# Optimization experiments

Hardware: AMD Instinct MI355X
Metric: run time of the kernel (lower is better)

The kernel has to match this reference:

```python
import jax, jax.numpy as jnp
import numpy as np

B, C_IN, C_OUT = 4, 64, 64
Z = H = W = 64
MZ = MH = MW = 16
R = 16


def setup_inputs() -> dict:
    key = jax.random.key(0)
    ks = jax.random.split(key, 12)
    p = lambda k, s: jax.random.normal(k, s, jnp.float32) * 0.02
    return {
        "x": jax.random.normal(ks[0], (B, C_IN, Z, H, W), jnp.float32),
        "U_in": p(ks[1], (C_IN, R)),
        "U_out": p(ks[2], (C_OUT, R)),
        "U_z": p(ks[3], (MZ, R)),
        "U_h": p(ks[4], (MH, R)),
        "U_w": p(ks[5], (MW, R)),
        "U_z2": p(ks[6], (MZ, R)),
        "U_h2": p(ks[7], (MH, R)),
        "core_r": p(ks[8], (R, R, R, R, R)),
        "core_i": p(ks[9], (R, R, R, R, R)),
        "core2_r": p(ks[10], (R, R, R, R, R)),
        "core2_i": p(ks[11], (R, R, R, R, R)),
    }


def _reconstruct(U_in, U_out, Uz, Uh, Uw, core):
    # Original: einsum('ir,or,zr,hr,wr,abcde->iozwh', ..., core).
    # core's a..e indices are summed independently of the shared r index,
    # so the weight equals the CP outer product scaled by core.sum().
    c = jnp.complex64
    w = jnp.einsum('ir,or,zr,hr,wr->iozwh',
                   U_in.astype(c), U_out.astype(c), Uz.astype(c),
                   Uh.astype(c), Uw.astype(c))
    return w * jnp.sum(core)  # (in, out, mz, mw, mh)


def reference(x, U_in, U_out, U_z, U_h, U_w, U_z2, U_h2,
              core_r, core_i, core2_r, core2_i):
    mz, mh, mw = U_z.shape[0], U_h.shape[0], U_w.shape[0]
    b, _, z, h, w = x.shape
    core = core_r + 1j * core_i
    core2 = core2_r + 1j * core2_i

    x_ft = jnp.fft.rfftn(x, axes=(-3, -2, -1))  # (B, Cin, Z, H, W//2+1) c64
    w1 = _reconstruct(U_in, U_out, U_z, U_h, U_w, core)
    w2 = _reconstruct(U_in, U_out, U_z2, U_h2, U_w, core2)

    lo = jnp.einsum('bixyz,ioxyz->boxyz', x_ft[:, :, :mz, :mh, :mw], w1)
    hi = jnp.einsum('bixyz,ioxyz->boxyz', x_ft[:, :, -mz:, :mh, :mw], w2)

    out_ft = jnp.zeros((b, U_out.shape[0], z, h, w // 2 + 1), jnp.complex64)
    out_ft = out_ft.at[:, :, :mz, :mh, :mw].set(lo)
    out_ft = out_ft.at[:, :, -mz:, :mh, :mw].set(hi)

    return jnp.fft.irfftn(out_ft, s=(z, h, w), axes=(-3, -2, -1)).astype(jnp.float32)
```

## Files before the change

### kernel.cpp

```cpp
#include <hip/hip_runtime.h>

#define TWOPI 6.28318530717958647692f

constexpr float COSQ[17] = {
  1.0f, 0.995184727f, 0.980785280f, 0.956940336f, 0.923879533f,
  0.881921264f, 0.831469612f, 0.773010453f, 0.707106781f,
  0.634393284f, 0.555570233f, 0.471396737f, 0.382683432f,
  0.290284677f, 0.195090322f, 0.098017140f, 0.0f
};
__host__ __device__ constexpr float cos64f(int k) {
  k &= 63;
  return (k <= 16) ? COSQ[k] : (k < 32) ? -COSQ[32 - k]
       : (k <= 48) ? -COSQ[k - 32] : COSQ[64 - k];
}
__host__ __device__ constexpr float sin64f(int k) { return cos64f(k + 48); }


__global__ __launch_bounds__(256) void k_core_partial(
    const float* __restrict__ a0, const float* __restrict__ a1,
    const float* __restrict__ a2, const float* __restrict__ a3,
    float* __restrict__ partial) {
  const float* p = blockIdx.y == 0 ? a0 : blockIdx.y == 1 ? a1
                 : blockIdx.y == 2 ? a2 : a3;
  const float4* p4 = (const float4*)p;
  float s = 0.f;
  int base = blockIdx.x * 4096 + threadIdx.x;
  #pragma unroll
  for (int i = 0; i < 16; ++i) {
    float4 v = p4[base + i * 256];
    s += (v.x + v.y) + (v.z + v.w);
  }
  __shared__ float red[256];
  red[threadIdx.x] = s;
  __syncthreads();
  for (int off = 128; off; off >>= 1) {
    if (threadIdx.x < off) red[threadIdx.x] += red[threadIdx.x + off];
    __syncthreads();
  }
  if (threadIdx.x == 0) partial[blockIdx.y * 64 + blockIdx.x] = red[0];
}

__global__ __launch_bounds__(256) void k_fwd_wh(const float* __restrict__ x,
                                                float2* __restrict__ A2) {
  __shared__ float2 T[4][64][17];
  int wave = threadIdx.x >> 6, lane = threadIdx.x & 63;
  int plane = blockIdx.x * 4 + wave;
  const float* xp = x + (size_t)plane * 4096 + lane;
  float cre[16], cim[16];
  {
    float x0 = xp[0], x32 = xp[32 * 64];
    #pragma unroll
    for (int hf = 0; hf < 16; ++hf) {
      cre[hf] = x0 + ((hf & 1) ? -x32 : x32);
      cim[hf] = 0.f;
    }
  }
  #pragma unroll
  for (int h = 1; h < 32; ++h) {
    float va = xp[h * 64], vb = xp[(64 - h) * 64];
    float u = va + vb, d = va - vb;
    #pragma unroll
    for (int hf = 0; hf < 16; ++hf) {
      cre[hf] = fmaf(u, cos64f(h * hf), cre[hf]);
      cim[hf] = fmaf(d, -sin64f(h * hf), cim[hf]);
    }
  }
  #pragma unroll
  for (int hf = 0; hf < 16; ++hf)
    T[wave][lane][hf] = make_float2(cre[hf], cim[hf]);
  __syncthreads();
  int hf = lane & 15, wq = lane >> 4;
  float2 rot[4], CS[4], acc[4];
  float2 T0 = T[wave][0][hf], T32 = T[wave][32][hf];
  #pragma unroll
  for (int j = 0; j < 4; ++j) {
    int wf = wq + 4 * j;
    float s, c;
    sincosf((TWOPI / 64.f) * (float)wf, &s, &c);
    rot[j] = make_float2(c, s);
    CS[j] = make_float2(c, s);
    float sgn = (wf & 1) ? -1.f : 1.f;
    acc[j] = make_float2(T0.x + sgn * T32.x, T0.y + sgn * T32.y);
  }
  #pragma unroll 4
  for (int w = 1; w < 32; ++w) {
    float2 a = T[wave][w][hf], b2 = T[wave][64 - w][hf];
    float Sr = a.x + b2.x, Si = a.y + b2.y;
    float Dr = a.x - b2.x, Di = a.y - b2.y;
    #pragma unroll
    for (int j = 0; j < 4; ++j) {
      float C = CS[j].x, Sn = CS[j].y;
      acc[j].x = fmaf(Sr, C, fmaf(Di, Sn, acc[j].x));
      acc[j].y = fmaf(Si, C, fmaf(-Dr, Sn, acc[j].y));
      float nC = C * rot[j].x - Sn * rot[j].y;
      CS[j].y = fmaf(C, rot[j].y, Sn * rot[j].x);
      CS[j].x = nC;
    }
  }
  float2* dst = A2 + (size_t)plane * 256 + lane;
  #pragma unroll
  for (int j = 0; j < 4; ++j) dst[j * 64] = acc[j];
}

__global__ __launch_bounds__(256) void k_proj(const float2* __restrict__ A2,
                                              float2* __restrict__ P,
                                              const float* __restrict__ U_in,
                                              const float* __restrict__ partial,
                                              float* __restrict__ S) {
  if (blockIdx.x == 0 && threadIdx.x < 4) {
    float s = 0.f;
    for (int j = 0; j < 64; ++j) s += partial[threadIdx.x * 64 + j];
    S[threadIdx.x] = s;
  }
  __shared__ float sU[1024];
  int t = threadIdx.x;
  #pragma unroll
  for (int i = 0; i < 4; ++i) sU[t + 256 * i] = U_in[t + 256 * i];
  __syncthreads();
  int b = blockIdx.x >> 6, z = blockIdx.x & 63;
  const float2* src = A2 + (((size_t)b * 64) * 64 + z) * 256 + t;
  float2 acc[16];
  #pragma unroll
  for (int r = 0; r < 16; ++r) acc[r] = make_float2(0.f, 0.f);
  for (int c = 0; c < 64; ++c) {
    float2 v = src[(size_t)c * 16384];
    #pragma unroll
    for (int r = 0; r < 16; ++r) {
      float u = sU[c * 16 + r];
      acc[r].x = fmaf(v.x, u, acc[r].x);
      acc[r].y = fmaf(v.y, u, acc[r].y);
    }
  }
  float2* dst = P + (((size_t)b * 16) * 64 + z) * 256 + t;
  #pragma unroll
  for (int r = 0; r < 16; ++r) dst[(size_t)r * 16384] = acc[r];
}

template <int HALF>
__device__ __forceinline__ void inv_z_body(const float* __restrict__ gr,
                                           const float* __restrict__ gi,
                                           float2* __restrict__ dst) {
  if (HALF == 0) {
    {
      float sr = 0.f, si = 0.f;
      #pragma unroll
      for (int k = 0; k < 32; ++k) { sr += gr[k]; si += gi[k]; }
      dst[0] = make_float2(sr, si);
    }
    #pragma unroll
    for (int z = 1; z <= 16; ++z) {
      float Ar = 0.f, Ai = 0.f, Br = 0.f, Bi = 0.f;
      #pragma unroll
      for (int k = 0; k < 32; ++k) {
        const int f = (k < 16) ? k : (k + 32);
        const float c = cos64f(z * f), s = sin64f(z * f);
        Ar = fmaf(gr[k], c, Ar); Ai = fmaf(gi[k], c, Ai);
        Br = fmaf(gr[k], s, Br); Bi = fmaf(gi[k], s, Bi);
      }
      dst[z * 256] = make_float2(Ar - Bi, Ai + Br);
      dst[(64 - z) * 256] = make_float2(Ar + Bi, Ai - Br);
    }
  } else {
    {
      float sr = 0.f, si = 0.f;
      #pragma unroll
      for (int k = 0; k < 32; ++k) {
        if (k & 1) { sr -= gr[k]; si -= gi[k]; }
        else       { sr += gr[k]; si += gi[k]; }
      }
      dst[32 * 256] = make_float2(sr, si);
    }
    #pragma unroll
    for (int z = 17; z < 32; ++z) {
      float Ar = 0.f, Ai = 0.f, Br = 0.f, Bi = 0.f;
      #pragma unroll
      for (int k = 0; k < 32; ++k) {
        const int f = (k < 16) ? k : (k + 32);
        const float c = cos64f(z * f), s = sin64f(z * f);
        Ar = fmaf(gr[k], c, Ar); Ai = fmaf(gi[k], c, Ai);
        Br = fmaf(gr[k], s, Br); Bi = fmaf(gi[k], s, Bi);
      }
      dst[z * 256] = make_float2(Ar - Bi, Ai + Br);
      dst[(64 - z) * 256] = make_float2(Ar + Bi, Ai - Br);
    }
  }
}

__global__ __launch_bounds__(256) void k_zmix(
    const float2* __restrict__ P, float2* __restrict__ Q,
    const float* __restrict__ U_z, const float* __restrict__ U_h,
    const float* __restrict__ U_w, const float* __restrict__ U_z2,
    const float* __restrict__ U_h2, const float* __restrict__ S4) {
  int br = blockIdx.x, r = br & 15, t = threadIdx.x;
  int hf = t & 15, wf = ((t >> 4) & 3) + 4 * (t >> 6);
  const float2* src = P + (size_t)br * 16384 + t;
  float2 acc[32];
  {
    float2 v0 = src[0], v32 = src[32 * 256];
    #pragma unroll
    for (int k = 0; k < 16; ++k) {
      float sgn = (k & 1) ? -1.f : 1.f;
      float2 e = make_float2(v0.x + sgn * v32.x, v0.y + sgn * v32.y);
      acc[k] = e;
      acc[k + 16] = e;
    }
  }
  #pragma unroll
  for (int z = 1; z < 32; ++z) {
    float2 a = src[z * 256], b = src[(64 - z) * 256];
    float Sr = a.x + b.x, Si = a.y + b.y;
    float Dr = a.x - b.x, Di = a.y - b.y;
    #pragma unroll
    for (int k = 0; k < 16; ++k) {
      {
        const float c = cos64f(z * k), s = sin64f(z * k);
        acc[k].x = fmaf(Sr, c, fmaf(Di, s, acc[k].x));
        acc[k].y = fmaf(Si, c, fmaf(-Dr, s, acc[k].y));
      }
      {
        const float c = cos64f(z * (k + 48)), s = sin64f(z * (k + 48));
        acc[k + 16].x = fmaf(Sr, c, fmaf(Di, s, acc[k + 16].x));
        acc[k + 16].y = fmaf(Si, c, fmaf(-Dr, s, acc[k + 16].y));
      }
    }
  }
  const float invN = 1.0f / 262144.0f;
  float S1r = S4[0] * invN, S1i = S4[1] * invN;
  float S2r = S4[2] * invN, S2i = S4[3] * invN;
  float cw = U_w[hf * 16 + r];
  float ch1 = U_h[wf * 16 + r] * cw, ch2 = U_h2[wf * 16 + r] * cw;
  float gr[32], gi[32];
  #pragma unroll
  for (int k = 0; k < 16; ++k) {
    float2 v = acc[k];
    float g = U_z[k * 16 + r] * ch1;
    float Fr = S1r * g, Fi = S1i * g;
    gr[k] = v.x * Fr - v.y * Fi;
    gi[k] = v.x * Fi + v.y * Fr;
  }
  #pragma unroll
  for (int k = 0; k < 16; ++k) {
    float2 v = acc[k + 16];
    float g = U_z2[k * 16 + r] * ch2;
    float Fr = S2r * g, Fi = S2i * g;
    gr[k + 16] = v.x * Fr - v.y * Fi;
    gi[k + 16] = v.x * Fi + v.y * Fr;
  }
  float2* dst = Q + (size_t)br * 16384 + t;
  if (blockIdx.y == 0) inv_z_body<0>(gr, gi, dst);
  else                 inv_z_body<1>(gr, gi, dst);
}

__global__ __launch_bounds__(256) void k_inv_hw_ex(
    const float2* __restrict__ Q, float* __restrict__ out,
    const float* __restrict__ U_out) {
  __shared__ float2 sQ[16][256];
  __shared__ float2 GLo[4][256];
  __shared__ float sU[1024];
  int t = threadIdx.x;
  int b = blockIdx.x >> 6, z = blockIdx.x & 63, og = blockIdx.y;
  #pragma unroll
  for (int i = 0; i < 4; ++i) sU[t + 256 * i] = U_out[t + 256 * i];
  #pragma unroll
  for (int r = 0; r < 16; ++r)
    sQ[r][t] = Q[((size_t)(b * 16 + r) * 64 + z) * 256 + t];
  __syncthreads();
  int wave = t >> 6, lane = t & 63;
  float2 E2[16];
  {
    float s, c;
    sincosf((TWOPI / 64.f) * (float)lane, &s, &c);
    float2 E = make_float2(c, s);
    float2 St = E;
    #pragma unroll
    for (int wfi = 1; wfi < 16; ++wfi) {
      E2[wfi] = make_float2(E.x + E.x, E.y + E.y);
      float ex = E.x * St.x - E.y * St.y;
      E.y = fmaf(E.x, St.y, E.y * St.x);
      E.x = ex;
    }
  }
  for (int oi = 0; oi < 8; ++oi) {
    int o = og * 32 + wave * 8 + oi;
    #pragma unroll
    for (int q = 0; q < 4; ++q) {
      int tt = lane + 64 * q;
      float re = 0.f, im = 0.f;
      #pragma unroll
      for (int r = 0; r < 16; ++r) {
        float u = sU[o * 16 + r];
        float2 v = sQ[r][tt];
        re = fmaf(v.x, u, re);
        im = fmaf(v.y, u, im);
      }
      GLo[wave][tt] = make_float2(re, im);
    }
    float qre[16], qim[16];
    #pragma unroll
    for (int hfi = 0; hfi < 16; ++hfi) {
      float2 g0 = GLo[wave][hfi];
      float ar = g0.x, ai = g0.y;
      #pragma unroll
      for (int wfi = 1; wfi < 16; ++wfi) {
        float2 gv = GLo[wave][(wfi >> 2) * 64 + (wfi & 3) * 16 + hfi];
        ar = fmaf(gv.x, E2[wfi].x, fmaf(-gv.y, E2[wfi].y, ar));
        ai = fmaf(gv.x, E2[wfi].y, fmaf(gv.y, E2[wfi].x, ai));
      }
      qre[hfi] = ar; qim[hfi] = ai;
    }
    float* op = out + (((size_t)(b * 64 + o) * 64 + z)) * 4096 + lane;
    {
      float Pv = qre[0];
      #pragma unroll
      for (int hfi = 1; hfi < 16; ++hfi) Pv += qre[hfi];
      op[0] = Pv;
    }
    {
      float Pv = qre[0];
      #pragma unroll
      for (int hfi = 1; hfi < 16; ++hfi)
        Pv += (hfi & 1) ? -qre[hfi] : qre[hfi];
      op[32 * 64] = Pv;
    }
    #pragma unroll
    for (int h = 1; h < 32; ++h) {
      float Pv = qre[0], Qv = 0.f;
      #pragma unroll
      for (int hfi = 1; hfi < 16; ++hfi) {
        Pv = fmaf(qre[hfi], cos64f(h * hfi), Pv);
        Qv = fmaf(qim[hfi], sin64f(h * hfi), Qv);
      }
      op[h * 64] = Pv - Qv;
      op[(64 - h) * 64] = Pv + Qv;
    }
  }
}

extern "C" void kernel_launch(void* const* d_in, const int* in_sizes, int n_in,
                              void* d_out, int out_size, void* d_ws,
                              size_t ws_size, hipStream_t stream) {
  const float* x    = (const float*)d_in[0];
  const float* Uin  = (const float*)d_in[1];
  const float* Uout = (const float*)d_in[2];
  const float* Uz   = (const float*)d_in[3];
  const float* Uh   = (const float*)d_in[4];
  const float* Uw   = (const float*)d_in[5];
  const float* Uz2  = (const float*)d_in[6];
  const float* Uh2  = (const float*)d_in[7];
  const float* cr   = (const float*)d_in[8];
  const float* ci   = (const float*)d_in[9];
  const float* c2r  = (const float*)d_in[10];
  const float* c2i  = (const float*)d_in[11];
  float* outp = (float*)d_out;

  char* ws = (char*)d_ws;
  float* S       = (float*)ws;
  float* partial = (float*)(ws + 256);
  float2* A2 = (float2*)(ws + 4096);
  float2* P  = (float2*)(ws + 33558528);
  float2* Q  = (float2*)(ws + 41947136);

  k_core_partial<<<dim3(64, 4), 256, 0, stream>>>(cr, ci, c2r, c2i, partial);
  k_fwd_wh<<<4096, 256, 0, stream>>>(x, A2);
  k_proj<<<256, 256, 0, stream>>>(A2, P, Uin, partial, S);
  k_zmix<<<dim3(64, 2), 256, 0, stream>>>(P, Q, Uz, Uh, Uw, Uz2, Uh2, S);
  k_inv_hw_ex<<<dim3(256, 2), 256, 0, stream>>>(Q, outp, Uout);
}
```

Baseline: 194.4 us.

## Fuse core reduction into forward FFT kernel and widen grids of later stages

Merges the core-sum reduction kernel into the forward W/H DFT kernel by assigning the first 256 blocks to the reduction, which removes one launch. It also doubles or quadruples the grids of the projection, z-mix and inverse kernels by splitting the rank, z-range and output-channel work across more blocks. The point is to fill more compute units on small stages, at the cost of redundant loads such as repeated reads of A2 and P and repeated zmix forward work per block.

```diff
diff --git a/kernel.cpp b/kernel.cpp
--- a/kernel.cpp
+++ b/kernel.cpp
@@ -16,35 +16,35 @@
 __host__ __device__ constexpr float sin64f(int k) { return cos64f(k + 48); }
 
 
-__global__ __launch_bounds__(256) void k_core_partial(
+__global__ __launch_bounds__(256) void k_fwd_wh_core(
+    const float* __restrict__ x, float2* __restrict__ A2,
     const float* __restrict__ a0, const float* __restrict__ a1,
     const float* __restrict__ a2, const float* __restrict__ a3,
     float* __restrict__ partial) {
-  const float* p = blockIdx.y == 0 ? a0 : blockIdx.y == 1 ? a1
-                 : blockIdx.y == 2 ? a2 : a3;
-  const float4* p4 = (const float4*)p;
-  float s = 0.f;
-  int base = blockIdx.x * 4096 + threadIdx.x;
-  #pragma unroll
-  for (int i = 0; i < 16; ++i) {
-    float4 v = p4[base + i * 256];
-    s += (v.x + v.y) + (v.z + v.w);
-  }
+  __shared__ float2 T[4][64][17];
   __shared__ float red[256];
-  red[threadIdx.x] = s;
-  __syncthreads();
-  for (int off = 128; off; off >>= 1) {
-    if (threadIdx.x < off) red[threadIdx.x] += red[threadIdx.x + off];
+  if (blockIdx.x < 256) {
+    int bx = blockIdx.x & 63, by = blockIdx.x >> 6;
+    const float* p = by == 0 ? a0 : by == 1 ? a1 : by == 2 ? a2 : a3;
+    const float4* p4 = (const float4*)p;
+    float s = 0.f;
+    int base = bx * 4096 + threadIdx.x;
+    #pragma unroll
+    for (int i = 0; i < 16; ++i) {
+      float4 v = p4[base + i * 256];
+      s += (v.x + v.y) + (v.z + v.w);
+    }
+    red[threadIdx.x] = s;
     __syncthreads();
-  }
-  if (threadIdx.x == 0) partial[blockIdx.y * 64 + blockIdx.x] = red[0];
-}
-
-__global__ __launch_bounds__(256) void k_fwd_wh(const float* __restrict__ x,
-                                                float2* __restrict__ A2) {
-  __shared__ float2 T[4][64][17];
+    for (int off = 128; off; off >>= 1) {
+      if (threadIdx.x < off) red[threadIdx.x] += red[threadIdx.x + off];
+      __syncthreads();
+    }
+    if (threadIdx.x == 0) partial[by * 64 + bx] = red[0];
+    return;
+  }
   int wave = threadIdx.x >> 6, lane = threadIdx.x & 63;
-  int plane = blockIdx.x * 4 + wave;
+  int plane = (blockIdx.x - 256) * 4 + wave;
   const float* xp = x + (size_t)plane * 4096 + lane;
   float cre[16], cim[16];
   {
@@ -107,7 +107,7 @@
                                               const float* __restrict__ U_in,
                                               const float* __restrict__ partial,
                                               float* __restrict__ S) {
-  if (blockIdx.x == 0 && threadIdx.x < 4) {
+  if (blockIdx.x == 0 && blockIdx.y == 0 && threadIdx.x < 4) {
     float s = 0.f;
     for (int j = 0; j < 64; ++j) s += partial[threadIdx.x * 64 + j];
     S[threadIdx.x] = s;
@@ -117,72 +117,58 @@
   #pragma unroll
   for (int i = 0; i < 4; ++i) sU[t + 256 * i] = U_in[t + 256 * i];
   __syncthreads();
-  int b = blockIdx.x >> 6, z = blockIdx.x & 63;
+  int b = blockIdx.x >> 6, z = blockIdx.x & 63, r0 = blockIdx.y * 8;
   const float2* src = A2 + (((size_t)b * 64) * 64 + z) * 256 + t;
-  float2 acc[16];
-  #pragma unroll
-  for (int r = 0; r < 16; ++r) acc[r] = make_float2(0.f, 0.f);
+  float2 acc[8];
+  #pragma unroll
+  for (int r = 0; r < 8; ++r) acc[r] = make_float2(0.f, 0.f);
   for (int c = 0; c < 64; ++c) {
     float2 v = src[(size_t)c * 16384];
     #pragma unroll
-    for (int r = 0; r < 16; ++r) {
-      float u = sU[c * 16 + r];
+    for (int r = 0; r < 8; ++r) {
+      float u = sU[c * 16 + r0 + r];
       acc[r].x = fmaf(v.x, u, acc[r].x);
       acc[r].y = fmaf(v.y, u, acc[r].y);
     }
   }
-  float2* dst = P + (((size_t)b * 16) * 64 + z) * 256 + t;
-  #pragma unroll
-  for (int r = 0; r < 16; ++r) dst[(size_t)r * 16384] = acc[r];
-}
-
-template <int HALF>
-__device__ __forceinline__ void inv_z_body(const float* __restrict__ gr,
-                                           const float* __restrict__ gi,
-                                           float2* __restrict__ dst) {
-  if (HALF == 0) {
-    {
-      float sr = 0.f, si = 0.f;
-      #pragma unroll
-      for (int k = 0; k < 32; ++k) { sr += gr[k]; si += gi[k]; }
-      dst[0] = make_float2(sr, si);
-    }
-    #pragma unroll
-    for (int z = 1; z <= 16; ++z) {
-      float Ar = 0.f, Ai = 0.f, Br = 0.f, Bi = 0.f;
-      #pragma unroll
-      for (int k = 0; k < 32; ++k) {
-        const int f = (k < 16) ? k : (k + 32);
-        const float c = cos64f(z * f), s = sin64f(z * f);
-        Ar = fmaf(gr[k], c, Ar); Ai = fmaf(gi[k], c, Ai);
-        Br = fmaf(gr[k], s, Br); Bi = fmaf(gi[k], s, Bi);
-      }
-      dst[z * 256] = make_float2(Ar - Bi, Ai + Br);
-      dst[(64 - z) * 256] = make_float2(Ar + Bi, Ai - Br);
-    }
-  } else {
-    {
-      float sr = 0.f, si = 0.f;
-      #pragma unroll
-      for (int k = 0; k < 32; ++k) {
-        if (k & 1) { sr -= gr[k]; si -= gi[k]; }
-        else       { sr += gr[k]; si += gi[k]; }
-      }
-      dst[32 * 256] = make_float2(sr, si);
-    }
-    #pragma unroll
-    for (int z = 17; z < 32; ++z) {
-      float Ar = 0.f, Ai = 0.f, Br = 0.f, Bi = 0.f;
-      #pragma unroll
-      for (int k = 0; k < 32; ++k) {
-        const int f = (k < 16) ? k : (k + 32);
-        const float c = cos64f(z * f), s = sin64f(z * f);
-        Ar = fmaf(gr[k], c, Ar); Ai = fmaf(gi[k], c, Ai);
-        Br = fmaf(gr[k], s, Br); Bi = fmaf(gi[k], s, Bi);
-      }
-      dst[z * 256] = make_float2(Ar - Bi, Ai + Br);
-      dst[(64 - z) * 256] = make_float2(Ar + Bi, Ai - Br);
-    }
+  float2* dst = P + (((size_t)b * 16 + r0) * 64 + z) * 256 + t;
+  #pragma unroll
+  for (int r = 0; r < 8; ++r) dst[(size_t)r * 16384] = acc[r];
+}
+
+template <int Y>
+__device__ __forceinline__ void inv_z_q(const float* __restrict__ gr,
+                                        const float* __restrict__ gi,
+                                        float2* __restrict__ dst) {
+  if (Y == 0) {
+    float sr = 0.f, si = 0.f;
+    #pragma unroll
+    for (int k = 0; k < 32; ++k) { sr += gr[k]; si += gi[k]; }
+    dst[0] = make_float2(sr, si);
+  }
+  if (Y == 2) {
+    float sr = 0.f, si = 0.f;
+    #pragma unroll
+    for (int k = 0; k < 32; ++k) {
+      if (k & 1) { sr -= gr[k]; si -= gi[k]; }
+      else       { sr += gr[k]; si += gi[k]; }
+    }
+    dst[32 * 256] = make_float2(sr, si);
+  }
+  constexpr int z0 = (Y == 0) ? 1 : (Y == 1) ? 9 : (Y == 2) ? 17 : 25;
+  constexpr int z1 = (Y == 0) ? 8 : (Y == 1) ? 16 : (Y == 2) ? 24 : 31;
+  #pragma unroll
+  for (int z = z0; z <= z1; ++z) {
+    float Ar = 0.f, Ai = 0.f, Br = 0.f, Bi = 0.f;
+    #pragma unroll
+    for (int k = 0; k < 32; ++k) {
+      const int f = (k < 16) ? k : (k + 32);
+      const float c = cos64f(z * f), s = sin64f(z * f);
+      Ar = fmaf(gr[k], c, Ar); Ai = fmaf(gi[k], c, Ai);
+      Br = fmaf(gr[k], s, Br); Bi = fmaf(gi[k], s, Bi);
+    }
+    dst[z * 256] = make_float2(Ar - Bi, Ai + Br);
+    dst[(64 - z) * 256] = make_float2(Ar + Bi, Ai - Br);
   }
 }
 
@@ -247,8 +233,12 @@
     gi[k + 16] = v.x * Fi + v.y * Fr;
   }
   float2* dst = Q + (size_t)br * 16384 + t;
-  if (blockIdx.y == 0) inv_z_body<0>(gr, gi, dst);
-  else                 inv_z_body<1>(gr, gi, dst);
+  switch (blockIdx.y) {
+    case 0: inv_z_q<0>(gr, gi, dst); break;
+    case 1: inv_z_q<1>(gr, gi, dst); break;
+    case 2: inv_z_q<2>(gr, gi, dst); break;
+    default: inv_z_q<3>(gr, gi, dst); break;
+  }
 }
 
 __global__ __launch_bounds__(256) void k_inv_hw_ex(
@@ -280,8 +270,8 @@
       E.x = ex;
     }
   }
-  for (int oi = 0; oi < 8; ++oi) {
-    int o = og * 32 + wave * 8 + oi;
+  for (int oi = 0; oi < 4; ++oi) {
+    int o = og * 16 + wave * 4 + oi;
     #pragma unroll
     for (int q = 0; q < 4; ++q) {
       int tt = lane + 64 * q;
@@ -360,9 +350,8 @@
   float2* P  = (float2*)(ws + 33558528);
   float2* Q  = (float2*)(ws + 41947136);
 
-  k_core_partial<<<dim3(64, 4), 256, 0, stream>>>(cr, ci, c2r, c2i, partial);
-  k_fwd_wh<<<4096, 256, 0, stream>>>(x, A2);
-  k_proj<<<256, 256, 0, stream>>>(A2, P, Uin, partial, S);
-  k_zmix<<<dim3(64, 2), 256, 0, stream>>>(P, Q, Uz, Uh, Uw, Uz2, Uh2, S);
-  k_inv_hw_ex<<<dim3(256, 2), 256, 0, stream>>>(Q, outp, Uout);
-}
+  k_fwd_wh_core<<<4352, 256, 0, stream>>>(x, A2, cr, ci, c2r, c2i, partial);
+  k_proj<<<dim3(256, 2), 256, 0, stream>>>(A2, P, Uin, partial, S);
+  k_zmix<<<dim3(64, 4), 256, 0, stream>>>(P, Q, Uz, Uh, Uw, Uz2, Uh2, S);
+  k_inv_hw_ex<<<dim3(256, 4), 256, 0, stream>>>(Q, outp, Uout);
+}
```

Measured after the change: 191.0 us. No clear change (-1.7%).
